# Optimization experiments

Hardware: AMD Instinct MI355X
Metric: run time of the kernel (lower is better)

Reference implementation:

```python
import jax, jax.numpy as jnp
import numpy as np

B, D, H = 8192, 256, 1024


def setup_inputs() -> dict:
    key = jax.random.key(0)
    ks = jax.random.split(key, 24)
    glorot = lambda k, o, i: jax.random.uniform(k, (o, i), jnp.float32, -1.0, 1.0) * jnp.sqrt(6.0 / (o + i))
    inp = {
        'x': jax.random.normal(ks[0], (B, D), jnp.float32),
        'm': (jax.random.uniform(ks[1], (B, D)) < 0.8).astype(jnp.float32),  # binary observation mask
        'delta': jax.random.uniform(ks[2], (B, D), jnp.float32),             # nonnegative time gaps
        'h': jax.random.normal(ks[3], (B, H), jnp.float32),
        'x_last_obs': jax.random.normal(ks[4], (B, D), jnp.float32),
        'x_mean': jax.random.normal(ks[5], (D,), jnp.float32),
        'W_gamma_x': jax.random.uniform(ks[6], (D,), jnp.float32, 0.001, 0.01),
        'b_gamma_x': jnp.zeros((D,), jnp.float32),
        'W_gamma_h': glorot(ks[7], H, D), 'b_gamma_h': jnp.zeros((H,), jnp.float32),
        'W_xz': glorot(ks[8], H, D), 'W_hz': glorot(ks[9], H, H),
        'W_mz': glorot(ks[10], H, D), 'b_mz': jnp.zeros((H,), jnp.float32),
        'W_xr': glorot(ks[11], H, D), 'W_hr': glorot(ks[12], H, H),
        'W_mr': glorot(ks[13], H, D), 'b_mr': jnp.zeros((H,), jnp.float32),
        'W_xh': glorot(ks[14], H, D), 'W_hh': glorot(ks[15], H, H),
        'W_mh': glorot(ks[16], H, D), 'b_mh': jnp.zeros((H,), jnp.float32),
    }
    return inp


def reference(x, m, delta, h, x_last_obs, x_mean,
              W_gamma_x, b_gamma_x, W_gamma_h, b_gamma_h,
              W_xz, W_hz, W_mz, b_mz,
              W_xr, W_hr, W_mr, b_mr,
              W_xh, W_hh, W_mh, b_mh):
    # input decay (per-feature) and hidden decay (linear of delta)
    gamma_x = jnp.exp(-jax.nn.relu(delta * W_gamma_x + b_gamma_x))        # [B, D]
    gamma_h = jnp.exp(-jax.nn.relu(delta @ W_gamma_h.T + b_gamma_h))     # [B, H]
    # imputation
    x_last_obs_new = jnp.where(m > 0, x, x_last_obs)
    x_imputed = gamma_x * x_last_obs_new + (1.0 - gamma_x) * x_mean
    x_hat = m * x + (1.0 - m) * x_imputed
    h_decayed = gamma_h * h
    # GRU gates (eval mode: no recurrent dropout)
    z = jax.nn.sigmoid(x_hat @ W_xz.T + h_decayed @ W_hz.T + m @ W_mz.T + b_mz)
    r = jax.nn.sigmoid(x_hat @ W_xr.T + h_decayed @ W_hr.T + m @ W_mr.T + b_mr)
    h_tilde = jnp.tanh(x_hat @ W_xh.T + (r * h_decayed) @ W_hh.T + m @ W_mh.T + b_mh)
    h_new = (1.0 - z) * h_decayed + z * h_tilde
    return h_new, x_last_obs_new
```

## Files before the change

### kernel.cpp

```cpp
#include <hip/hip_runtime.h>
#include <cstdint>
#include <cstddef>

typedef unsigned short u16;
typedef __attribute__((ext_vector_type(8))) short s16x8;
typedef __attribute__((ext_vector_type(8))) u16 u16x8;
typedef __attribute__((ext_vector_type(4))) float f32x4;

#define DEV static __device__ __forceinline__
#define GPTR(p) (const __attribute__((address_space(1))) void*)(p)
#define LPTR(p) (__attribute__((address_space(3))) void*)(p)

DEV float b2f(u16 u) { union { unsigned i; float f; } c; c.i = ((unsigned)u) << 16; return c.f; }
DEV u16 f2b(float f) {
  union { float f; unsigned i; } c; c.f = f;
  unsigned r = (c.i + 0x7fffu + ((c.i >> 16) & 1u)) >> 16;
  return (u16)r;
}
DEV float sigm(float x) { return 1.0f / (1.0f + __expf(-x)); }

__global__ __launch_bounds__(256) void pack_w(
    const float* __restrict__ Wxz, const float* __restrict__ Whz, const float* __restrict__ Wmz,
    const float* __restrict__ Wxr, const float* __restrict__ Whr, const float* __restrict__ Wmr,
    const float* __restrict__ Wxh, const float* __restrict__ Whh, const float* __restrict__ Wmh,
    const float* __restrict__ Wgh,
    u16* __restrict__ WZR, u16* __restrict__ WH, u16* __restrict__ WGH)
{
  int t = blockIdx.x * 256 + threadIdx.x;
  const float* src;
  u16* dst;
  if (t < 589824) {
    int row = t / 192;
    int col = (t % 192) * 8;
    int rr = row & 1023;
    const float *wx, *wh, *wm;
    if (row < 1024)      { wx = Wxz; wh = Whz; wm = Wmz; }
    else if (row < 2048) { wx = Wxr; wh = Whr; wm = Wmr; }
    else                 { wx = Wxh; wh = Whh; wm = Wmh; }
    if (col < 256)       src = wx + rr * 256 + col;
    else if (col < 1280) src = wh + (size_t)rr * 1024 + (col - 256);
    else                 src = wm + rr * 256 + (col - 1280);
    dst = (row < 2048) ? (WZR + (size_t)row * 1536 + col)
                       : (WH + (size_t)(row - 2048) * 1536 + col);
  } else {
    int t2 = t - 589824;
    src = Wgh + t2 * 8;
    dst = WGH + t2 * 8;
  }
  f32x4 a = *(const f32x4*)src;
  f32x4 b = *(const f32x4*)(src + 4);
  u16x8 v;
#pragma unroll
  for (int j = 0; j < 4; ++j) { v[j] = f2b(a[j]); v[j + 4] = f2b(b[j]); }
  *(u16x8*)dst = v;
}

__global__ __launch_bounds__(256) void elem_k(
    const float* __restrict__ x, const float* __restrict__ m, const float* __restrict__ delta,
    const float* __restrict__ xlo, const float* __restrict__ x_mean,
    const float* __restrict__ Wgx, const float* __restrict__ bgx,
    u16* __restrict__ X1, u16* __restrict__ Dbf,
    float* __restrict__ out_xlo)
{
  int t = blockIdx.x * 256 + threadIdx.x;
  int row = t >> 5;
  int col = (t & 31) * 8;
  size_t base = (size_t)row * 256 + col;
  u16x8 vxhat, vm16, vd16;
  f32x4 vlnew[2];
#pragma unroll
  for (int half = 0; half < 2; ++half) {
    f32x4 vx = *(const f32x4*)(x + base + half * 4);
    f32x4 vm = *(const f32x4*)(m + base + half * 4);
    f32x4 vd = *(const f32x4*)(delta + base + half * 4);
    f32x4 vl = *(const f32x4*)(xlo + base + half * 4);
    f32x4 vmean = *(const f32x4*)(x_mean + col + half * 4);
    f32x4 vwg = *(const f32x4*)(Wgx + col + half * 4);
    f32x4 vbg = *(const f32x4*)(bgx + col + half * 4);
#pragma unroll
    for (int j = 0; j < 4; ++j) {
      float mf = vm[j];
      float lnew = (mf > 0.5f) ? vx[j] : vl[j];
      vlnew[half][j] = lnew;
      float gx = __expf(-fmaxf(vd[j] * vwg[j] + vbg[j], 0.0f));
      float ximp = gx * lnew + (1.0f - gx) * vmean[j];
      float xhat = mf * vx[j] + (1.0f - mf) * ximp;
      vxhat[half * 4 + j] = f2b(xhat);
      vm16[half * 4 + j] = f2b(mf);
      vd16[half * 4 + j] = f2b(vd[j]);
    }
  }
  size_t r1536 = (size_t)row * 1536;
  *(u16x8*)(X1 + r1536 + col) = vxhat;
  *(u16x8*)(X1 + r1536 + 1280 + col) = vm16;
  *(u16x8*)(Dbf + base) = vd16;
  *(f32x4*)(out_xlo + base) = vlnew[0];
  *(f32x4*)(out_xlo + base + 4) = vlnew[1];
}

template<int EPI, int MF>
__global__ __launch_bounds__(512, 2) void gemm_bt(
    const u16* __restrict__ A, const u16* __restrict__ A2, int K,
    const u16* __restrict__ W,
    const float* __restrict__ bias0, const float* __restrict__ bias1,
    const float* __restrict__ auxf,
    const u16* __restrict__ auxb,
    const u16* __restrict__ aux2b,
    u16* __restrict__ out0b,
    u16* __restrict__ out1b,
    float* __restrict__ outf)
{
  constexpr int BM = MF * 32;
  constexpr int GX = (MF == 8) ? 8 : 4;
  constexpr int AL = MF / 4;
  constexpr int NPH = MF / 2;
  __shared__ alignas(16) u16 As[2][2][BM * 32];
  __shared__ alignas(16) u16 Bs[2][2][256 * 32];

  const int tid = threadIdx.x;
  const int lane = tid & 63;
  const int wave = tid >> 6;
  const int wr = wave >> 2;
  const int wc = wave & 3;

  const int d = blockIdx.y * GX + blockIdx.x;
  const int L = ((d & 7) << 5) | (d >> 3);
  const int brow = (L / GX) * BM;
  const int bcol = (L % GX) * 256;
  const int NT = K / 64;

  const int lr = lane & 15, g4 = lane >> 4;
  const int rchunk = ((g4 ^ ((lr >> 1) & 3)) * 8);
  const int sr16 = lane >> 2;
  const int scs = (lane & 3) ^ ((sr16 >> 1) & 3);

  f32x4 acc[MF][4];
#pragma unroll
  for (int i = 0; i < MF; ++i)
#pragma unroll
    for (int j = 0; j < 4; ++j) { f32x4 z0 = {0.f, 0.f, 0.f, 0.f}; acc[i][j] = z0; }

  auto stA = [&](int st, int bu, int kh) {
    int stc = st < NT ? st : NT - 1;
    const u16* Ab; size_t Astr; int co;
    if constexpr (EPI == 2) {
      if (stc >= 4 && stc < 20) { Ab = A2; Astr = 1024; co = stc * 64 + kh * 32 - 256; }
      else                      { Ab = A;  Astr = 1536; co = stc * 64 + kh * 32; }
    } else { Ab = A; Astr = (size_t)K; co = stc * 64 + kh * 32; }
#pragma unroll
    for (int q = 0; q < AL; ++q) {
      int rb = (q * 8 + wave) * 16;
      __builtin_amdgcn_global_load_lds(
          GPTR(Ab + (size_t)(brow + rb + sr16) * Astr + co + scs * 8),
          LPTR(&As[bu][kh][rb * 32]), 16, 0, 0);
    }
  };
  auto stB = [&](int st, int bu, int kh) {
    int stc = st < NT ? st : NT - 1;
    int co = stc * 64 + kh * 32;
#pragma unroll
    for (int q = 0; q < 2; ++q) {
      int rb = (q * 8 + wave) * 16;
      __builtin_amdgcn_global_load_lds(
          GPTR(W + (size_t)(bcol + rb + sr16) * (size_t)K + co + scs * 8),
          LPTR(&Bs[bu][kh][rb * 32]), 16, 0, 0);
    }
  };

  stA(0, 0, 0); stB(0, 0, 0);
  stA(0, 0, 1); stB(0, 0, 1);
  stA(1, 1, 0); stB(1, 1, 0);
  if constexpr (MF == 8) asm volatile("s_waitcnt vmcnt(8)" ::: "memory");
  else                   asm volatile("s_waitcnt vmcnt(6)" ::: "memory");
  __builtin_amdgcn_s_barrier();

  s16x8 bfr[4];
  for (int kt = 0; kt < NT; ++kt) {
    const int bu = kt & 1;
#pragma unroll
    for (int ph = 0; ph < NPH; ++ph) {
      const int ks = (MF == 8) ? (ph >> 1) : ph;
      const int mq = (MF == 8) ? (ph & 1) : 0;
      s16x8 af[4];
      if (mq == 0)
#pragma unroll
        for (int j = 0; j < 4; ++j)
          bfr[j] = *(const s16x8*)&Bs[bu][ks][(wc * 64 + j * 16 + lr) * 32 + rchunk];
#pragma unroll
      for (int ii = 0; ii < 4; ++ii)
        af[ii] = *(const s16x8*)&As[bu][ks][(wr * (BM / 2) + mq * 64 + ii * 16 + lr) * 32 + rchunk];
      if constexpr (MF == 8) {
        if (ph == 0)      stA(kt + 1, bu ^ 1, 1);
        else if (ph == 1) stB(kt + 1, bu ^ 1, 1);
        else if (ph == 2) stA(kt + 2, bu, 0);
        else              stB(kt + 2, bu, 0);
      } else {
        if (ph == 0) { stA(kt + 1, bu ^ 1, 1); stB(kt + 1, bu ^ 1, 1); }
        else         { stA(kt + 2, bu, 0);     stB(kt + 2, bu, 0); }
      }
      if constexpr (MF == 8) {
        if (ph & 1) asm volatile("s_waitcnt vmcnt(8)" ::: "memory");
      } else {
        asm volatile("s_waitcnt vmcnt(6)" ::: "memory");
      }
      __builtin_amdgcn_s_barrier();
      asm volatile("s_waitcnt lgkmcnt(0)" ::: "memory");
      __builtin_amdgcn_sched_barrier(0);
      __builtin_amdgcn_s_setprio(1);
#pragma unroll
      for (int ii = 0; ii < 4; ++ii)
#pragma unroll
        for (int j = 0; j < 4; ++j)
          acc[mq * 4 + ii][j] = __builtin_amdgcn_mfma_f32_16x16x32_bf16(
              af[ii], bfr[j], acc[mq * 4 + ii][j], 0, 0, 0);
      __builtin_amdgcn_s_setprio(0);
      __builtin_amdgcn_s_barrier();
    }
  }

  const int row0 = brow + wr * (MF * 16) + g4 * 4;
  const int col0 = bcol + wc * 64 + lr;
#pragma unroll
  for (int i = 0; i < MF; ++i) {
#pragma unroll
    for (int j = 0; j < 4; ++j) {
      int c_ = col0 + j * 16;
#pragma unroll
      for (int q = 0; q < 4; ++q) {
        int r_ = row0 + i * 16 + q;
        float v = acc[i][j][q];
        if constexpr (EPI == 0) {
          float p = v + bias0[c_];
          float gh = __expf(-fmaxf(p, 0.0f));
          float hd = gh * auxf[(size_t)r_ * 1024 + c_];
          out0b[(size_t)r_ * 1536 + 256 + c_] = f2b(hd);
        } else if constexpr (EPI == 1) {
          if (c_ < 1024) {
            out0b[(size_t)r_ * 1024 + c_] = f2b(sigm(v + bias0[c_]));
          } else {
            int jc = c_ - 1024;
            float rg = sigm(v + bias1[jc]);
            float hd = b2f(auxb[(size_t)r_ * 1536 + 256 + jc]);
            out1b[(size_t)r_ * 1024 + jc] = f2b(rg * hd);
          }
        } else {
          float ht = tanhf(v + bias0[c_]);
          float zz = b2f(aux2b[(size_t)r_ * 1024 + c_]);
          float hd = b2f(auxb[(size_t)r_ * 1536 + 256 + c_]);
          outf[(size_t)r_ * 1024 + c_] = (1.0f - zz) * hd + zz * ht;
        }
      }
    }
  }
}

extern "C" void kernel_launch(void* const* d_in, const int* in_sizes, int n_in,
                              void* d_out, int out_size, void* d_ws, size_t ws_size,
                              hipStream_t stream)
{
  const float* x     = (const float*)d_in[0];
  const float* m     = (const float*)d_in[1];
  const float* delta = (const float*)d_in[2];
  const float* h     = (const float*)d_in[3];
  const float* xlo   = (const float*)d_in[4];
  const float* xmean = (const float*)d_in[5];
  const float* Wgx   = (const float*)d_in[6];
  const float* bgx   = (const float*)d_in[7];
  const float* Wgh   = (const float*)d_in[8];
  const float* bgh   = (const float*)d_in[9];
  const float* Wxz   = (const float*)d_in[10];
  const float* Whz   = (const float*)d_in[11];
  const float* Wmz   = (const float*)d_in[12];
  const float* bmz   = (const float*)d_in[13];
  const float* Wxr   = (const float*)d_in[14];
  const float* Whr   = (const float*)d_in[15];
  const float* Wmr   = (const float*)d_in[16];
  const float* bmr   = (const float*)d_in[17];
  const float* Wxh   = (const float*)d_in[18];
  const float* Whh   = (const float*)d_in[19];
  const float* Wmh   = (const float*)d_in[20];
  const float* bmh   = (const float*)d_in[21];

  u16* X1  = (u16*)d_ws;
  u16* Z   = X1 + (size_t)8192 * 1536;
  u16* RH  = Z  + (size_t)8192 * 1024;
  u16* WZR = RH + (size_t)8192 * 1024;
  u16* WH  = WZR + (size_t)2048 * 1536;
  u16* Dbf = WH + (size_t)1024 * 1536;
  u16* WGH = Dbf + (size_t)8192 * 256;

  float* out_h   = (float*)d_out;
  float* out_xlo = out_h + (size_t)8192 * 1024;

  pack_w<<<2432, 256, 0, stream>>>(Wxz, Whz, Wmz, Wxr, Whr, Wmr, Wxh, Whh, Wmh, Wgh, WZR, WH, WGH);
  elem_k<<<1024, 256, 0, stream>>>(x, m, delta, xlo, xmean, Wgx, bgx, X1, Dbf, out_xlo);
  gemm_bt<0, 4><<<dim3(4, 64), 512, 0, stream>>>(
      Dbf, nullptr, 256, WGH, bgh, nullptr, h, nullptr, nullptr, X1, nullptr, nullptr);
  gemm_bt<1, 8><<<dim3(8, 32), 512, 0, stream>>>(
      X1, nullptr, 1536, WZR, bmz, bmr, nullptr, X1, nullptr, Z, RH, nullptr);
  gemm_bt<2, 4><<<dim3(4, 64), 512, 0, stream>>>(
      X1, RH, 1536, WH, bmh, nullptr, nullptr, X1, Z, nullptr, nullptr, out_h);
}
```

Measured before the change: 172.4 us.

## Software-pipeline LDS fragment loads to overlap with MFMA phases in GEMM

Restructures the GEMM main loop so LDS fragment reads for the next phase are issued right after the current phase's MFMAs. Each phase then computes on registers loaded earlier, which hides LDS latency behind matrix math. It uses double-buffered register fragments, splits MF=4 into half-width B fragments, and retunes vmcnt waits and barrier placement. In exchange it raises register pressure, and the hand-tuned wait counts risk being subtly wrong.

```diff
diff --git a/kernel.cpp b/kernel.cpp
--- a/kernel.cpp
+++ b/kernel.cpp
@@ -10,6 +10,9 @@
 #define DEV static __device__ __forceinline__
 #define GPTR(p) (const __attribute__((address_space(1))) void*)(p)
 #define LPTR(p) (__attribute__((address_space(3))) void*)(p)
+#define LGKM0 asm volatile("s_waitcnt lgkmcnt(0)" ::: "memory")
+#define SCHEDB __builtin_amdgcn_sched_barrier(0)
+#define BAR __builtin_amdgcn_s_barrier()
 
 DEV float b2f(u16 u) { union { unsigned i; float f; } c; c.i = ((unsigned)u) << 16; return c.f; }
 DEV u16 f2b(float f) {
@@ -113,7 +116,6 @@
   constexpr int BM = MF * 32;
   constexpr int GX = (MF == 8) ? 8 : 4;
   constexpr int AL = MF / 4;
-  constexpr int NPH = MF / 2;
   __shared__ alignas(16) u16 As[2][2][BM * 32];
   __shared__ alignas(16) u16 Bs[2][2][256 * 32];
 
@@ -166,55 +168,105 @@
           LPTR(&Bs[bu][kh][rb * 32]), 16, 0, 0);
     }
   };
+  auto LDA4 = [&](s16x8* dst, int bu, int ks, int mq) {
+#pragma unroll
+    for (int ii = 0; ii < 4; ++ii)
+      dst[ii] = *(const s16x8*)&As[bu][ks][(wr * (BM / 2) + mq * 64 + ii * 16 + lr) * 32 + rchunk];
+  };
+  auto LDB4 = [&](s16x8* dst, int bu, int ks) {
+#pragma unroll
+    for (int j = 0; j < 4; ++j)
+      dst[j] = *(const s16x8*)&Bs[bu][ks][(wc * 64 + j * 16 + lr) * 32 + rchunk];
+  };
+  auto LDB2 = [&](s16x8* dst, int bu, int ks, int nh) {
+#pragma unroll
+    for (int j = 0; j < 2; ++j)
+      dst[j] = *(const s16x8*)&Bs[bu][ks][(wc * 64 + nh * 32 + j * 16 + lr) * 32 + rchunk];
+  };
+  auto MM16 = [&](s16x8* a, s16x8* b, int mq) {
+#pragma unroll
+    for (int ii = 0; ii < 4; ++ii)
+#pragma unroll
+      for (int j = 0; j < 4; ++j)
+        acc[mq * 4 + ii][j] = __builtin_amdgcn_mfma_f32_16x16x32_bf16(
+            a[ii], b[j], acc[mq * 4 + ii][j], 0, 0, 0);
+  };
+  auto MM8 = [&](s16x8* a, s16x8* b, int nh) {
+#pragma unroll
+    for (int ii = 0; ii < 4; ++ii)
+#pragma unroll
+      for (int j = 0; j < 2; ++j)
+        acc[ii][nh * 2 + j] = __builtin_amdgcn_mfma_f32_16x16x32_bf16(
+            a[ii], b[j], acc[ii][nh * 2 + j], 0, 0, 0);
+  };
 
   stA(0, 0, 0); stB(0, 0, 0);
   stA(0, 0, 1); stB(0, 0, 1);
   stA(1, 1, 0); stB(1, 1, 0);
+  SCHEDB;
   if constexpr (MF == 8) asm volatile("s_waitcnt vmcnt(8)" ::: "memory");
   else                   asm volatile("s_waitcnt vmcnt(6)" ::: "memory");
-  __builtin_amdgcn_s_barrier();
-
-  s16x8 bfr[4];
-  for (int kt = 0; kt < NT; ++kt) {
-    const int bu = kt & 1;
-#pragma unroll
-    for (int ph = 0; ph < NPH; ++ph) {
-      const int ks = (MF == 8) ? (ph >> 1) : ph;
-      const int mq = (MF == 8) ? (ph & 1) : 0;
-      s16x8 af[4];
-      if (mq == 0)
-#pragma unroll
-        for (int j = 0; j < 4; ++j)
-          bfr[j] = *(const s16x8*)&Bs[bu][ks][(wc * 64 + j * 16 + lr) * 32 + rchunk];
-#pragma unroll
-      for (int ii = 0; ii < 4; ++ii)
-        af[ii] = *(const s16x8*)&As[bu][ks][(wr * (BM / 2) + mq * 64 + ii * 16 + lr) * 32 + rchunk];
-      if constexpr (MF == 8) {
-        if (ph == 0)      stA(kt + 1, bu ^ 1, 1);
-        else if (ph == 1) stB(kt + 1, bu ^ 1, 1);
-        else if (ph == 2) stA(kt + 2, bu, 0);
-        else              stB(kt + 2, bu, 0);
-      } else {
-        if (ph == 0) { stA(kt + 1, bu ^ 1, 1); stB(kt + 1, bu ^ 1, 1); }
-        else         { stA(kt + 2, bu, 0);     stB(kt + 2, bu, 0); }
-      }
-      if constexpr (MF == 8) {
-        if (ph & 1) asm volatile("s_waitcnt vmcnt(8)" ::: "memory");
-      } else {
-        asm volatile("s_waitcnt vmcnt(6)" ::: "memory");
-      }
-      __builtin_amdgcn_s_barrier();
-      asm volatile("s_waitcnt lgkmcnt(0)" ::: "memory");
-      __builtin_amdgcn_sched_barrier(0);
-      __builtin_amdgcn_s_setprio(1);
-#pragma unroll
-      for (int ii = 0; ii < 4; ++ii)
-#pragma unroll
-        for (int j = 0; j < 4; ++j)
-          acc[mq * 4 + ii][j] = __builtin_amdgcn_mfma_f32_16x16x32_bf16(
-              af[ii], bfr[j], acc[mq * 4 + ii][j], 0, 0, 0);
-      __builtin_amdgcn_s_setprio(0);
-      __builtin_amdgcn_s_barrier();
+  BAR;
+
+  if constexpr (MF == 8) {
+    s16x8 af0[4], af1[4], bf0[4], bf1[4];
+    LDA4(af0, 0, 0, 0); LDB4(bf0, 0, 0);
+    for (int kt = 0; kt < NT; ++kt) {
+      const int bu = kt & 1;
+      LGKM0; SCHEDB;
+      __builtin_amdgcn_s_setprio(1); MM16(af0, bf0, 0); __builtin_amdgcn_s_setprio(0);
+      LDA4(af1, bu, 0, 1);
+      stA(kt + 1, bu ^ 1, 1);
+      SCHEDB;
+      asm volatile("s_waitcnt vmcnt(6)" ::: "memory");
+      BAR;
+      LGKM0; SCHEDB;
+      __builtin_amdgcn_s_setprio(1); MM16(af1, bf0, 1); __builtin_amdgcn_s_setprio(0);
+      LDB4(bf1, bu, 1); LDA4(af0, bu, 1, 0);
+      stB(kt + 1, bu ^ 1, 1);
+      BAR;
+      LGKM0; SCHEDB;
+      __builtin_amdgcn_s_setprio(1); MM16(af0, bf1, 0); __builtin_amdgcn_s_setprio(0);
+      LDA4(af1, bu, 1, 1);
+      stA(kt + 2, bu, 0);
+      SCHEDB;
+      asm volatile("s_waitcnt vmcnt(6)" ::: "memory");
+      BAR;
+      LGKM0; SCHEDB;
+      __builtin_amdgcn_s_setprio(1); MM16(af1, bf1, 1); __builtin_amdgcn_s_setprio(0);
+      if (kt + 1 < NT) { LDB4(bf0, bu ^ 1, 0); LDA4(af0, bu ^ 1, 0, 0); }
+      stB(kt + 2, bu, 0);
+      BAR;
+    }
+  } else {
+    s16x8 af0[4], af1[4], bfA[2], bfB[2], bfC[2], bfD[2];
+    LDA4(af0, 0, 0, 0); LDB2(bfA, 0, 0, 0);
+    for (int kt = 0; kt < NT; ++kt) {
+      const int bu = kt & 1;
+      LGKM0; SCHEDB;
+      __builtin_amdgcn_s_setprio(1); MM8(af0, bfA, 0); __builtin_amdgcn_s_setprio(0);
+      LDB2(bfB, bu, 0, 1);
+      stA(kt + 1, bu ^ 1, 1);
+      SCHEDB;
+      asm volatile("s_waitcnt vmcnt(4)" ::: "memory");
+      BAR;
+      LGKM0; SCHEDB;
+      __builtin_amdgcn_s_setprio(1); MM8(af0, bfB, 1); __builtin_amdgcn_s_setprio(0);
+      LDA4(af1, bu, 1, 0); LDB2(bfC, bu, 1, 0);
+      stB(kt + 1, bu ^ 1, 1);
+      BAR;
+      LGKM0; SCHEDB;
+      __builtin_amdgcn_s_setprio(1); MM8(af1, bfC, 0); __builtin_amdgcn_s_setprio(0);
+      LDB2(bfD, bu, 1, 1);
+      stA(kt + 2, bu, 0);
+      SCHEDB;
+      asm volatile("s_waitcnt vmcnt(4)" ::: "memory");
+      BAR;
+      LGKM0; SCHEDB;
+      __builtin_amdgcn_s_setprio(1); MM8(af1, bfD, 1); __builtin_amdgcn_s_setprio(0);
+      if (kt + 1 < NT) { LDA4(af0, bu ^ 1, 0, 0); LDB2(bfA, bu ^ 1, 0, 0); }
+      stB(kt + 2, bu, 0);
+      BAR;
     }
   }
 
```

New measurement: 179.9 us. 1.04x slower.
